# Kernel optimization log

Measured on AMD Instinct MI355X. Metric: run time of the kernel, lower is better.

The kernel has to match this reference:

```python
import jax, jax.numpy as jnp
import numpy as np

LN_EPS = 1e-5
COS_EPS2 = 1e-16  # torch cosine_similarity: (n1*n2).clamp_min(eps**2), eps=1e-8


def _ln(x, g, b):
    m = jnp.mean(x, -1, keepdims=True)
    v = jnp.mean((x - m) ** 2, -1, keepdims=True)
    return (x - m) * jax.lax.rsqrt(v + LN_EPS) * g + b


def _span_pool(x, starts, ends, word_length):
    # x: [B, S, D] (text_feat[:, 1:]); spans pooled into slots 1..S of a [B, S+1, D] buffer
    B, S, D = x.shape
    cs = jnp.concatenate([jnp.zeros((B, 1, D), x.dtype), jnp.cumsum(x, axis=1)], axis=1)  # [B, S+1, D]
    pool = (jnp.take_along_axis(cs, ends[..., None], axis=1)
            - jnp.take_along_axis(cs, starts[..., None], axis=1))  # [B, S, D]
    mask = (jnp.arange(S)[None, :] < word_length[:, None]).astype(x.dtype)[..., None]
    return jnp.pad(pool * mask, ((0, 0), (1, 0), (0, 0)))  # [B, S+1, D], slot 0 = zeros


def _forward(text_hidden, vit_feature, pooler_out, target_mask, adj,
             ln_g, ln_b, wq, wk, wv, fc_w, mha_ln_g, mha_ln_b,
             w1a, b1a, w1b, b1b, w2a, b2a, w2b, b2b,
             loc_w, loc_b, out_w, out_b, word_length, tran_indices):
    B, L, D = text_hidden.shape
    H = wq.shape[1] // D  # n_head=4, d_k=d_v=768

    # eval mode: all dropouts are identity
    text_feat = _ln(text_hidden, ln_g, ln_b)

    # MultiHeadAttention(text_feat, vit, vit)
    q = (text_feat @ wq).reshape(B, L, H, D)
    k = (vit_feature @ wk).reshape(B, -1, H, D)
    v = (vit_feature @ wv).reshape(B, -1, H, D)
    attn = jnp.einsum('blhd,bmhd->bhlm', q, k) / jnp.sqrt(jnp.asarray(D, text_feat.dtype))
    attn = jax.nn.softmax(attn, axis=-1)
    ctx = jnp.einsum('bhlm,bmhd->blhd', attn, v).reshape(B, L, H * D)
    text_include_img = _ln(ctx @ fc_w + text_feat, mha_ln_g, mha_ln_b)

    # pairwise cosine similarity over sequence positions: [B, L, L]
    n = jnp.linalg.norm(text_include_img, axis=-1)
    sim = jnp.einsum('bld,bmd->blm', text_include_img, text_include_img)
    sim = sim / jnp.maximum(n[:, :, None] * n[:, None, :], COS_EPS2)

    global_bert = _ln(pooler_out, ln_g, ln_b)

    # span pooling of subword features into word slots (tmps buffers)
    starts, ends = tran_indices[..., 0], tran_indices[..., 1]
    tmps = _span_pool(text_feat[:, 1:, :], starts, ends, word_length)
    tmps_ti = _span_pool(text_include_img[:, 1:, :], starts, ends, word_length)

    adj_ti = adj * sim
    den = jnp.sum(adj, axis=2, keepdims=True) + 1.0
    den_ti = jnp.sum(adj_ti, axis=2, keepdims=True) + 1.0

    # NOTE: original loop recomputes from tmps each layer and only keeps the last
    # iteration, so only W1[-1]/W2[-1] affect the output (faithfully reproduced).
    g_dep = jax.nn.relu(((adj @ tmps) @ w1b + b1b) / den)
    g_ti = jax.nn.relu(((adj_ti @ tmps_ti) @ w2b + b2b) / den_ti)

    asp_wn = jnp.sum(target_mask, axis=1, keepdims=True)  # [B, 1]
    m = target_mask[:, :, None]
    gcn_out_text = jnp.sum(g_dep * m, axis=1) / asp_wn
    gcn_out_ti = jnp.sum(g_ti * m, axis=1) / asp_wn

    local_feat = jnp.concatenate([gcn_out_text, gcn_out_ti], axis=1) @ loc_w + loc_b
    feat = jnp.concatenate([global_bert, local_feat], axis=1)
    return feat @ out_w + out_b


def setup_inputs():
    key = jax.random.key(0)
    ks = jax.random.split(key, 20)
    B, L, NV, D, H, NC = 64, 160, 197, 768, 4, 3
    S = L - 1
    s = 0.02
    text_hidden = jax.random.normal(ks[0], (B, L, D), jnp.float32)
    vit_feature = jax.random.normal(ks[1], (B, NV, D), jnp.float32)
    pooler_out = jax.random.normal(ks[2], (B, D), jnp.float32)
    adj = jax.random.uniform(ks[3], (B, L, L), jnp.float32)
    target_mask = jnp.zeros((B, L), jnp.float32).at[:, 1:9].set(1.0)
    word_length = jax.random.randint(ks[4], (B,), 1, S, jnp.int32)
    lens = jax.random.randint(ks[5], (B, S), 1, 3, jnp.int32)  # 1-2 subtokens per word
    cum = jnp.cumsum(lens, axis=1)
    ends = jnp.minimum(cum, S)
    starts = jnp.minimum(cum - lens, S)
    tran_indices = jnp.stack([starts, ends], axis=-1).astype(jnp.int32)
    return dict(
        text_hidden=text_hidden, vit_feature=vit_feature, pooler_out=pooler_out,
        target_mask=target_mask, adj=adj,
        ln_g=jnp.ones((D,), jnp.float32), ln_b=jnp.zeros((D,), jnp.float32),
        wq=jax.random.normal(ks[6], (D, H * D), jnp.float32) * s,
        wk=jax.random.normal(ks[7], (D, H * D), jnp.float32) * s,
        wv=jax.random.normal(ks[8], (D, H * D), jnp.float32) * s,
        fc_w=jax.random.normal(ks[9], (H * D, D), jnp.float32) * s,
        mha_ln_g=jnp.ones((D,), jnp.float32), mha_ln_b=jnp.zeros((D,), jnp.float32),
        w1a=jax.random.normal(ks[10], (D, D), jnp.float32) * s, b1a=jnp.zeros((D,), jnp.float32),
        w1b=jax.random.normal(ks[11], (D, D), jnp.float32) * s, b1b=jnp.zeros((D,), jnp.float32),
        w2a=jax.random.normal(ks[12], (D, D), jnp.float32) * s, b2a=jnp.zeros((D,), jnp.float32),
        w2b=jax.random.normal(ks[13], (D, D), jnp.float32) * s, b2b=jnp.zeros((D,), jnp.float32),
        loc_w=jax.random.normal(ks[14], (2 * D, D), jnp.float32) * s, loc_b=jnp.zeros((D,), jnp.float32),
        out_w=jax.random.normal(ks[15], (2 * D, NC), jnp.float32) * s, out_b=jnp.zeros((NC,), jnp.float32),
        word_length=word_length, tran_indices=tran_indices,
    )


def reference(text_hidden, vit_feature, pooler_out, target_mask, adj,
              ln_g, ln_b, wq, wk, wv, fc_w, mha_ln_g, mha_ln_b,
              w1a, b1a, w1b, b1b, w2a, b2a, w2b, b2b,
              loc_w, loc_b, out_w, out_b, word_length, tran_indices):
    return _forward(text_hidden, vit_feature, pooler_out, target_mask, adj,
                    ln_g, ln_b, wq, wk, wv, fc_w, mha_ln_g, mha_ln_b,
                    w1a, b1a, w1b, b1b, w2a, b2a, w2b, b2b,
                    loc_w, loc_b, out_w, out_b, word_length, tran_indices)
```

## Files before the change

kernel.cpp:

```cpp
#include <hip/hip_runtime.h>
#include <math.h>

#define BB 64
#define LL 160
#define DD 768
#define HH 4
#define NVV 197
#define SS 159

typedef unsigned short u16;
typedef __attribute__((ext_vector_type(8))) short bf16x8;
typedef __attribute__((ext_vector_type(4))) float f32x4;

union QU { uint4 u; bf16x8 v; };

__device__ __forceinline__ u16 f2bf(float a) {
  unsigned u = __builtin_bit_cast(unsigned, a);
  u = (u + 0x7FFFu + ((u >> 16) & 1u)) >> 16;
  return (u16)u;
}
__device__ __forceinline__ unsigned f2bf2(float a, float b) {
  return (unsigned)f2bf(a) | ((unsigned)f2bf(b) << 16);
}
__device__ __forceinline__ float bf2f(u16 h) {
  unsigned u = ((unsigned)h) << 16;
  return __builtin_bit_cast(float, u);
}
__device__ __forceinline__ float to_f(float x) { return x; }
__device__ __forceinline__ float to_f(u16 x) { return bf2f(x); }

__device__ __forceinline__ void async16(const u16* g, void* l) {
  __builtin_amdgcn_global_load_lds(
      (const __attribute__((address_space(1))) void*)g,
      (__attribute__((address_space(3))) void*)l, 16, 0, 0);
}

__device__ __forceinline__ uint4 load_bf8(const u16* __restrict__ P, long long rowbase,
                                          int valid, int kb, int K) {
  uint4 r;
  if (valid && (kb + 8 <= K) && (((rowbase + kb) & 7) == 0)) {
    r = *(const uint4*)(P + rowbase + kb);
  } else {
    u16 e[8];
    #pragma unroll
    for (int i = 0; i < 8; ++i) { int k = kb + i; e[i] = (valid && k < K) ? P[rowbase + k] : (u16)0; }
    r.x = e[0] | ((unsigned)e[1] << 16); r.y = e[2] | ((unsigned)e[3] << 16);
    r.z = e[4] | ((unsigned)e[5] << 16); r.w = e[6] | ((unsigned)e[7] << 16);
  }
  return r;
}

__device__ __forceinline__ uint4 load_row8(const float* __restrict__ P, long long rowbase,
                                           int valid_row, int kb, int K) {
  float f[8];
  if (valid_row && (kb + 8 <= K)) {
    const float4* p0 = (const float4*)(P + rowbase + kb);
    float4 x = p0[0], y = p0[1];
    f[0] = x.x; f[1] = x.y; f[2] = x.z; f[3] = x.w;
    f[4] = y.x; f[5] = y.y; f[6] = y.z; f[7] = y.w;
  } else {
    #pragma unroll
    for (int e = 0; e < 8; ++e) { int k = kb + e; f[e] = (valid_row && k < K) ? P[rowbase + k] : 0.f; }
  }
  uint4 r;
  r.x = f2bf2(f[0], f[1]); r.y = f2bf2(f[2], f[3]);
  r.z = f2bf2(f[4], f[5]); r.w = f2bf2(f[6], f[7]);
  return r;
}

__device__ __forceinline__ uint4 load_a(const u16* P, long long rb, int v, int kb, int K) {
  return load_bf8(P, rb, v, kb, K);
}
__device__ __forceinline__ uint4 load_a(const float* P, long long rb, int v, int kb, int K) {
  return load_row8(P, rb, v, kb, K);
}

template<int DUAL>
__global__ __launch_bounds__(256) void gemm97(
    const u16* __restrict__ A0, const u16* __restrict__ B0m,
    float* __restrict__ Cf0, u16* __restrict__ Cb0,
    const u16* __restrict__ A1, const u16* __restrict__ B1m,
    float* __restrict__ Cf1, u16* __restrict__ Cb1,
    int M, int N, int K, int lda, int ldb, int ldc, int nbx,
    const float* __restrict__ bias0, const float* __restrict__ bias1,
    const u16* __restrict__ resid0,
    const float* __restrict__ rowdiv0, const float* __restrict__ rowdiv1,
    int relu) {
  __shared__ uint4 Al[2][4][128];
  __shared__ uint4 Bl[2][4][128];

  int id = blockIdx.x;
  int nset = gridDim.x >> DUAL;
  int setid = DUAL ? (id >= nset ? 1 : 0) : 0;
  if (setid) id -= nset;
  const u16* A = setid ? A1 : A0;
  const u16* Bm = setid ? B1m : B0m;
  float* Cf = setid ? Cf1 : Cf0;
  u16* Cb = setid ? Cb1 : Cb0;
  const float* bias = setid ? bias1 : bias0;
  const float* rowdiv = setid ? rowdiv1 : rowdiv0;
  const u16* residB = setid ? (const u16*)nullptr : resid0;

  int qq = nset >> 3, rr = nset & 7;
  int xcd = id & 7, idx = id >> 3;
  int swz = (xcd < rr ? xcd * (qq + 1) : rr * (qq + 1) + (xcd - rr) * qq) + idx;
  int bx = swz % nbx, by = swz / nbx;
  int row0 = by * 128, col0 = bx * 128;

  int t = threadIdx.x, l = t & 63, w = t >> 6;
  int wr = (w >> 1) * 64, wc = (w & 1) * 64;
  int li = l & 15, kg = l >> 4;
  int nt = K >> 5;

  const u16* Ap0 = A + (long long)(row0 + l) * lda + w * 8;
  const u16* Ap1 = A + (long long)(row0 + 64 + l) * lda + w * 8;
  const u16* Bp0 = Bm + (long long)(col0 + l) * ldb + w * 8;
  const u16* Bp1 = Bm + (long long)(col0 + 64 + l) * ldb + w * 8;

  f32x4 acc[4][4] = {};

  auto STAGE = [&](int kt, int bi) {
    long long ko = (long long)kt << 5;
    async16(Ap0 + ko, &Al[bi][w][0]);
    async16(Ap1 + ko, &Al[bi][w][64]);
    async16(Bp0 + ko, &Bl[bi][w][0]);
    async16(Bp1 + ko, &Bl[bi][w][64]);
  };

  STAGE(0, 0);
  __syncthreads();
  int buf = 0;
  for (int kt = 0; kt < nt; ++kt) {
    if (kt + 1 < nt) STAGE(kt + 1, buf ^ 1);
    QU a[4], b[4];
    #pragma unroll
    for (int i = 0; i < 4; ++i) a[i].u = Al[buf][kg][wr + i * 16 + li];
    #pragma unroll
    for (int j = 0; j < 4; ++j) b[j].u = Bl[buf][kg][wc + j * 16 + li];
    __builtin_amdgcn_s_setprio(1);
    #pragma unroll
    for (int i = 0; i < 4; ++i)
      #pragma unroll
      for (int j = 0; j < 4; ++j)
        acc[i][j] = __builtin_amdgcn_mfma_f32_16x16x32_bf16(a[i].v, b[j].v, acc[i][j], 0, 0, 0);
    __builtin_amdgcn_s_setprio(0);
    __syncthreads();
    buf ^= 1;
  }

  #pragma unroll
  for (int i = 0; i < 4; ++i)
    #pragma unroll
    for (int j = 0; j < 4; ++j) {
      int col = col0 + wc + j * 16 + li;
      float bv = bias ? bias[col] : 0.f;
      #pragma unroll
      for (int r = 0; r < 4; ++r) {
        int row = row0 + wr + i * 16 + kg * 4 + r;
        long long ci = (long long)row * ldc + col;
        float v = acc[i][j][r] + bv;
        if (residB) v += bf2f(residB[ci]);
        if (rowdiv) v /= rowdiv[row];
        if (relu) v = fmaxf(v, 0.f);
        if (Cf) Cf[ci] = v;
        if (Cb) Cb[ci] = f2bf(v);
      }
    }
}

template<bool TRANSB, typename TA>
__global__ __launch_bounds__(256) void gemm_bf16(
    const TA* __restrict__ A, const u16* __restrict__ Bm,
    float* __restrict__ Cf, u16* __restrict__ Cb,
    int M, int N, int K, int lda, int ldb, int ldc, int Hb,
    long long sAb, long long sAh, long long sBb, long long sBh,
    long long sCb, long long sCh,
    float alpha, const float* __restrict__ bias) {
  int bb = blockIdx.z / Hb, hh = blockIdx.z % Hb;
  A += bb * sAb + hh * sAh;
  Bm += bb * sBb + hh * sBh;
  long long coff = bb * sCb + hh * sCh;

  __shared__ uint4 As4[4][64];
  __shared__ uint4 Bs4[4][64];

  int row0 = blockIdx.y * 64, col0 = blockIdx.x * 64;
  int t = threadIdx.x;
  int l = t & 63, w = t >> 6;
  int mq = (w >> 1) * 32, nq = (w & 1) * 32;

  int am = t >> 2, akq = t & 3;
  int bn = t & 63, bkq = t >> 6;

  f32x4 acc[2][2] = {};

  for (int k0 = 0; k0 < K; k0 += 32) {
    As4[akq][am] = load_a(A, (long long)(row0 + am) * lda, (row0 + am) < M, k0 + akq * 8, K);
    if (TRANSB) {
      Bs4[akq][am] = load_bf8(Bm, (long long)(col0 + am) * ldb, (col0 + am) < N, k0 + akq * 8, K);
    } else {
      int gn = col0 + bn;
      u16 e[8];
      #pragma unroll
      for (int i = 0; i < 8; ++i) {
        int k = k0 + bkq * 8 + i;
        e[i] = (gn < N && k < K) ? Bm[(long long)k * ldb + gn] : (u16)0;
      }
      uint4 r;
      r.x = e[0] | ((unsigned)e[1] << 16); r.y = e[2] | ((unsigned)e[3] << 16);
      r.z = e[4] | ((unsigned)e[5] << 16); r.w = e[6] | ((unsigned)e[7] << 16);
      Bs4[bkq][bn] = r;
    }
    __syncthreads();
    int kg = l >> 4, li = l & 15;
    QU a0, a1, b0, b1;
    a0.u = As4[kg][mq + li];
    a1.u = As4[kg][mq + 16 + li];
    b0.u = Bs4[kg][nq + li];
    b1.u = Bs4[kg][nq + 16 + li];
    acc[0][0] = __builtin_amdgcn_mfma_f32_16x16x32_bf16(a0.v, b0.v, acc[0][0], 0, 0, 0);
    acc[0][1] = __builtin_amdgcn_mfma_f32_16x16x32_bf16(a0.v, b1.v, acc[0][1], 0, 0, 0);
    acc[1][0] = __builtin_amdgcn_mfma_f32_16x16x32_bf16(a1.v, b0.v, acc[1][0], 0, 0, 0);
    acc[1][1] = __builtin_amdgcn_mfma_f32_16x16x32_bf16(a1.v, b1.v, acc[1][1], 0, 0, 0);
    __syncthreads();
  }

  #pragma unroll
  for (int i = 0; i < 2; ++i) {
    #pragma unroll
    for (int j = 0; j < 2; ++j) {
      int colj = col0 + nq + j * 16 + (l & 15);
      float bv = (bias && colj < N) ? bias[colj] : 0.f;
      #pragma unroll
      for (int r = 0; r < 4; ++r) {
        int gr = row0 + mq + i * 16 + (l >> 4) * 4 + r;
        if (gr < M && colj < N) {
          long long ci = coff + (long long)gr * ldc + colj;
          float v = acc[i][j][r] * alpha + bv;
          if (Cf) Cf[ci] = v;
          if (Cb) Cb[ci] = f2bf(v);
        }
      }
    }
  }
}

__global__ __launch_bounds__(256) void sim_kernel(
    const u16* __restrict__ TII, const float* __restrict__ nrm,
    const float* __restrict__ adjf, u16* __restrict__ adjtiB) {
  int bb = blockIdx.z;
  const u16* T = TII + (long long)bb * LL * DD;

  __shared__ uint4 As4[4][64];
  __shared__ uint4 Bs4[4][64];

  int row0 = blockIdx.y * 64, col0 = blockIdx.x * 64;
  int t = threadIdx.x;
  int l = t & 63, w = t >> 6;
  int mq = (w >> 1) * 32, nq = (w & 1) * 32;
  int am = t >> 2, akq = t & 3;

  f32x4 acc[2][2] = {};

  for (int k0 = 0; k0 < DD; k0 += 32) {
    As4[akq][am] = load_bf8(T, (long long)(row0 + am) * DD, (row0 + am) < LL, k0 + akq * 8, DD);
    Bs4[akq][am] = load_bf8(T, (long long)(col0 + am) * DD, (col0 + am) < LL, k0 + akq * 8, DD);
    __syncthreads();
    int kg = l >> 4, li = l & 15;
    QU a0, a1, b0, b1;
    a0.u = As4[kg][mq + li];
    a1.u = As4[kg][mq + 16 + li];
    b0.u = Bs4[kg][nq + li];
    b1.u = Bs4[kg][nq + 16 + li];
    acc[0][0] = __builtin_amdgcn_mfma_f32_16x16x32_bf16(a0.v, b0.v, acc[0][0], 0, 0, 0);
    acc[0][1] = __builtin_amdgcn_mfma_f32_16x16x32_bf16(a0.v, b1.v, acc[0][1], 0, 0, 0);
    acc[1][0] = __builtin_amdgcn_mfma_f32_16x16x32_bf16(a1.v, b0.v, acc[1][0], 0, 0, 0);
    acc[1][1] = __builtin_amdgcn_mfma_f32_16x16x32_bf16(a1.v, b1.v, acc[1][1], 0, 0, 0);
    __syncthreads();
  }

  #pragma unroll
  for (int i = 0; i < 2; ++i) {
    #pragma unroll
    for (int j = 0; j < 2; ++j) {
      int colj = col0 + nq + j * 16 + (l & 15);
      #pragma unroll
      for (int r = 0; r < 4; ++r) {
        int gr = row0 + mq + i * 16 + (l >> 4) * 4 + r;
        if (gr < LL && colj < LL) {
          float nl = nrm[bb * LL + gr], nm = nrm[bb * LL + colj];
          long long ai = ((long long)bb * LL + gr) * LL + colj;
          float s = acc[i][j][r] / fmaxf(nl * nm, 1e-16f);
          adjtiB[ai] = f2bf(adjf[ai] * s);
        }
      }
    }
  }
}

__device__ __forceinline__ float block_sum(float v, float* sm) {
  #pragma unroll
  for (int o = 32; o > 0; o >>= 1) v += __shfl_down(v, o);
  int lane = threadIdx.x & 63, w = threadIdx.x >> 6;
  if (lane == 0) sm[w] = v;
  __syncthreads();
  if (threadIdx.x == 0) sm[0] = sm[0] + sm[1] + sm[2] + sm[3];
  __syncthreads();
  float r = sm[0];
  __syncthreads();
  return r;
}

__global__ __launch_bounds__(256) void ln_kernel(const float* __restrict__ x, float* __restrict__ yf,
                                                 u16* __restrict__ yb,
                                                 const float* __restrict__ g, const float* __restrict__ b,
                                                 float* __restrict__ nrmout) {
  __shared__ float sm[4];
  long long row = blockIdx.x;
  const float* xr = x + row * DD;
  int t = threadIdx.x;
  float v0 = xr[t], v1 = xr[t + 256], v2 = xr[t + 512];
  float s = block_sum(v0 + v1 + v2, sm);
  float m = s * (1.f / 768.f);
  float d0 = v0 - m, d1 = v1 - m, d2 = v2 - m;
  float vv = block_sum(d0 * d0 + d1 * d1 + d2 * d2, sm);
  float rstd = rsqrtf(vv * (1.f / 768.f) + 1e-5f);
  float y0 = d0 * rstd * g[t] + b[t];
  float y1 = d1 * rstd * g[t + 256] + b[t + 256];
  float y2 = d2 * rstd * g[t + 512] + b[t + 512];
  if (yf) { float* yr = yf + row * DD; yr[t] = y0; yr[t + 256] = y1; yr[t + 512] = y2; }
  if (yb) { u16* yr = yb + row * DD; yr[t] = f2bf(y0); yr[t + 256] = f2bf(y1); yr[t + 512] = f2bf(y2); }
  if (nrmout) {
    float s2 = block_sum(y0 * y0 + y1 * y1 + y2 * y2, sm);
    if (t == 0) nrmout[row] = sqrtf(s2);
  }
}

__global__ __launch_bounds__(256) void softmax_bf16(u16* __restrict__ SP, int nrows) {
  int row = blockIdx.x * 4 + (threadIdx.x >> 6);
  int lane = threadIdx.x & 63;
  if (row >= nrows) return;
  u16* ar = SP + (long long)row * 200;
  float vals[4];
  float mx = -1e30f;
  int cnt = 0;
  for (int i = lane; i < NVV; i += 64) { float v = bf2f(ar[i]); vals[cnt++] = v; mx = fmaxf(mx, v); }
  #pragma unroll
  for (int o = 32; o > 0; o >>= 1) mx = fmaxf(mx, __shfl_xor(mx, o));
  float sum = 0.f;
  for (int j = 0; j < cnt; ++j) { vals[j] = __expf(vals[j] - mx); sum += vals[j]; }
  #pragma unroll
  for (int o = 32; o > 0; o >>= 1) sum += __shfl_xor(sum, o);
  float inv = 1.f / sum;
  cnt = 0;
  for (int i = lane; i < NVV; i += 64) ar[i] = f2bf(vals[cnt++] * inv);
  for (int i = NVV + lane; i < 200; i += 64) ar[i] = 0;
}

template<typename T>
__global__ __launch_bounds__(256) void pool_kernel(const T* __restrict__ src, u16* __restrict__ dst,
                                                   const int* __restrict__ wl, const int* __restrict__ tran) {
  int b = blockIdx.x, i = blockIdx.y, d = threadIdx.x;
  long long ob = ((long long)b * LL + i) * DD;
  float r0 = 0.f, r1 = 0.f, r2 = 0.f;
  if (i > 0 && (i - 1) < wl[b]) {
    int w = i - 1;
    int st = tran[(b * SS + w) * 2];
    int en = tran[(b * SS + w) * 2 + 1];
    const T* sb = src + (long long)b * LL * DD;
    for (int s = st; s < en; ++s) {
      const T* rp = sb + (long long)(1 + s) * DD;
      r0 += to_f(rp[d]); r1 += to_f(rp[d + 256]); r2 += to_f(rp[d + 512]);
    }
  }
  dst[ob + d] = f2bf(r0);
  dst[ob + d + 256] = f2bf(r1);
  dst[ob + d + 512] = f2bf(r2);
}

__global__ __launch_bounds__(256) void den_kernel(const float* __restrict__ adjf, const u16* __restrict__ atB,
                                                  float* __restrict__ den, float* __restrict__ den_ti) {
  __shared__ float sm[4];
  int bl = blockIdx.x, m = threadIdx.x;
  float a = 0.f, at = 0.f;
  if (m < LL) {
    long long idx = (long long)bl * LL + m;
    a = adjf[idx];
    at = bf2f(atB[idx]);
  }
  float sa = block_sum(a, sm);
  float sat = block_sum(at, sm);
  if (m == 0) { den[bl] = sa + 1.f; den_ti[bl] = sat + 1.f; }
}

__global__ __launch_bounds__(256) void gcn_kernel(const u16* __restrict__ g, const float* __restrict__ mask,
                                                  u16* __restrict__ outB, int coloff) {
  int b = blockIdx.x;
  int d = blockIdx.y * 256 + threadIdx.x;
  float s = 0.f, wn = 0.f;
  for (int l = 0; l < LL; ++l) {
    float mk = mask[b * LL + l];
    wn += mk;
    s += mk * bf2f(g[((long long)b * LL + l) * DD + d]);
  }
  outB[(long long)b * (2 * DD) + coloff + d] = f2bf(s / wn);
}

__global__ __launch_bounds__(256) void final_kernel(const float* __restrict__ gb, const float* __restrict__ lf,
                                                    const float* __restrict__ ow, const float* __restrict__ ob,
                                                    float* __restrict__ out) {
  __shared__ float sm[4];
  int b = blockIdx.x / 3, c = blockIdx.x % 3;
  int t = threadIdx.x;
  float s = 0.f;
  for (int k = t; k < DD; k += 256) {
    s += gb[b * DD + k] * ow[k * 3 + c];
    s += lf[b * DD + k] * ow[(DD + k) * 3 + c];
  }
  float tot = block_sum(s, sm);
  if (t == 0) out[b * 3 + c] = tot + ob[c];
}

__global__ __launch_bounds__(256) void conv_kernel(const float4* __restrict__ x, uint2* __restrict__ y, int n4) {
  int i = blockIdx.x * 256 + threadIdx.x;
  if (i < n4) {
    float4 v = x[i];
    uint2 o;
    o.x = f2bf2(v.x, v.y);
    o.y = f2bf2(v.z, v.w);
    y[i] = o;
  }
}

__global__ __launch_bounds__(256) void tconv_kernel(const float* __restrict__ src, u16* __restrict__ dst,
                                                    int R, int C, int lds, int ldd) {
  __shared__ float sm[32][33];
  int t = threadIdx.x;
  int tx = t & 31, ty8 = t >> 5;
  int r0 = blockIdx.y * 32, c0 = blockIdx.x * 32;
  for (int i = ty8; i < 32; i += 8) {
    int r = r0 + i, c = c0 + tx;
    sm[i][tx] = (r < R && c < C) ? src[(long long)r * lds + c] : 0.f;
  }
  __syncthreads();
  for (int i = ty8; i < 32; i += 8) {
    int c = c0 + i, r = r0 + tx;
    if (c < C && r < R) dst[(long long)c * ldd + r] = f2bf(sm[tx][i]);
  }
}

__global__ __launch_bounds__(256) void vtrans_kernel(const u16* __restrict__ src, u16* __restrict__ dst) {
  __shared__ u16 sm[32][33];
  int b = blockIdx.z;
  int c0 = blockIdx.x * 32;
  int r0 = blockIdx.y * 32;
  int t = threadIdx.x, tx = t & 31, ty8 = t >> 5;
  const u16* sb = src + (long long)b * NVV * DD;
  for (int i = ty8; i < 32; i += 8) {
    int r = r0 + i, c = c0 + tx;
    sm[i][tx] = (r < NVV && c < DD) ? sb[(long long)r * DD + c] : (u16)0;
  }
  __syncthreads();
  u16* db = dst + (long long)b * DD * 208;
  for (int i = ty8; i < 32; i += 8) {
    int j = c0 + i, k = r0 + tx;
    if (j < DD && k < 208) db[(long long)j * 208 + k] = sm[tx][i];
  }
}

template<typename TA>
static void gemm(hipStream_t s, bool transb, const TA* A, const u16* B, float* Cf, u16* Cb,
                 int M, int N, int K, int lda, int ldb, int ldc, int batches, int Hb,
                 long long sAb, long long sAh, long long sBb, long long sBh,
                 long long sCb, long long sCh, float alpha, const float* bias) {
  dim3 g((N + 63) / 64, (M + 63) / 64, batches);
  if (transb)
    gemm_bf16<true, TA><<<g, 256, 0, s>>>(A, B, Cf, Cb, M, N, K, lda, ldb, ldc, Hb,
                                          sAb, sAh, sBb, sBh, sCb, sCh, alpha, bias);
  else
    gemm_bf16<false, TA><<<g, 256, 0, s>>>(A, B, Cf, Cb, M, N, K, lda, ldb, ldc, Hb,
                                           sAb, sAh, sBb, sBh, sCb, sCh, alpha, bias);
}

extern "C" void kernel_launch(void* const* d_in, const int* in_sizes, int n_in,
                              void* d_out, int out_size, void* d_ws, size_t ws_size,
                              hipStream_t stream) {
  const float* text_hidden = (const float*)d_in[0];
  const float* vit_feature = (const float*)d_in[1];
  const float* pooler_out = (const float*)d_in[2];
  const float* target_mask = (const float*)d_in[3];
  const float* adj = (const float*)d_in[4];
  const float* ln_g = (const float*)d_in[5];
  const float* ln_b = (const float*)d_in[6];
  const float* wq = (const float*)d_in[7];
  const float* wk = (const float*)d_in[8];
  const float* wv = (const float*)d_in[9];
  const float* fc_w = (const float*)d_in[10];
  const float* mha_ln_g = (const float*)d_in[11];
  const float* mha_ln_b = (const float*)d_in[12];
  const float* w1b = (const float*)d_in[15];
  const float* b1b = (const float*)d_in[16];
  const float* w2b = (const float*)d_in[19];
  const float* b2b = (const float*)d_in[20];
  const float* loc_w = (const float*)d_in[21];
  const float* loc_b = (const float*)d_in[22];
  const float* out_w = (const float*)d_in[23];
  const float* out_b = (const float*)d_in[24];
  const int* word_length = (const int*)d_in[25];
  const int* tran = (const int*)d_in[26];
  float* out = (float*)d_out;

  const long long BLD = (long long)BB * LL * DD;
  const long long BND = (long long)BB * NVV * DD;
  const long long WHD = (long long)768 * 768;
  const long long W3K = (long long)768 * 3072;

  char* base = (char*)d_ws;
  auto alloc = [&](size_t bytes) { char* p = base; base += (bytes + 255) & ~(size_t)255; return p; };

  float* R_ACC = (float*)alloc(BLD * 4);
  u16* TFB = (u16*)alloc(BLD * 2);
  u16* vitB = (u16*)alloc(BND * 2);
  u16* BIG = (u16*)alloc((size_t)4 * BLD * 2);
  u16* Mt = (u16*)alloc((size_t)4 * WHD * 2);
  u16* Wvf = (u16*)alloc((size_t)4 * WHD * 2);
  u16* SH = (u16*)alloc((size_t)BB * HH * LL * 200 * 2);
  u16* adjtiB = (u16*)alloc((size_t)BB * LL * LL * 2);
  u16* w1bT = (u16*)alloc(WHD * 2);
  u16* w2bT = (u16*)alloc(WHD * 2);
  u16* locT = (u16*)alloc((size_t)768 * 1536 * 2);
  u16* linB = (u16*)alloc((size_t)BB * 1536 * 2);
  float* nrm = (float*)alloc((size_t)BB * LL * 4);
  float* den = (float*)alloc((size_t)BB * LL * 4);
  float* den_ti = (float*)alloc((size_t)BB * LL * 4);
  float* global_bert = (float*)alloc((size_t)BB * DD * 4);
  float* local_feat = (float*)alloc((size_t)BB * DD * 4);

  u16* wqB = BIG;
  u16* wkB = BIG + W3K;
  u16* wvB = BIG + 2 * W3K;
  u16* fcT = BIG + 3 * W3K;
  u16* T2PV = BIG;
  u16* TIIB = BIG + 2 * BLD;
  u16* tmpsTiB = BIG;
  u16* g2B = BIG + BLD;
  u16* S4 = SH;
  u16* H1 = SH;
  u16* tmpsB = vitB;
  u16* h2B = TFB;
  u16* g1B = vitB;
  u16* vitT = (u16*)R_ACC;

  const float inv_sqrt_d = 1.0f / sqrtf((float)DD);
  const long long sA_L = (long long)LL * DD;

  {
    int n4v = (int)(BND / 4);
    conv_kernel<<<(n4v + 255) / 256, 256, 0, stream>>>((const float4*)vit_feature, (uint2*)vitB, n4v);
    vtrans_kernel<<<dim3(24, 7, BB), 256, 0, stream>>>(vitB, vitT);
    int n4w = (int)(W3K / 4);
    conv_kernel<<<(n4w + 255) / 256, 256, 0, stream>>>((const float4*)wq, (uint2*)wqB, n4w);
    conv_kernel<<<(n4w + 255) / 256, 256, 0, stream>>>((const float4*)wk, (uint2*)wkB, n4w);
    conv_kernel<<<(n4w + 255) / 256, 256, 0, stream>>>((const float4*)wv, (uint2*)wvB, n4w);
    for (int h = 0; h < HH; ++h)
      tconv_kernel<<<dim3(24, 24), 256, 0, stream>>>(fc_w + (size_t)h * WHD, fcT + (size_t)h * WHD,
                                                     768, 768, 768, 768);
    tconv_kernel<<<dim3(24, 24), 256, 0, stream>>>(w1b, w1bT, 768, 768, 768, 768);
    tconv_kernel<<<dim3(24, 24), 256, 0, stream>>>(w2b, w2bT, 768, 768, 768, 768);
    tconv_kernel<<<dim3(24, 48), 256, 0, stream>>>(loc_w, locT, 1536, 768, 768, 1536);
    gemm<u16>(stream, true, wkB, wqB, nullptr, Mt, 768, 768, 768, 3072, 3072, 768,
              HH, 1, 768, 0, 768, 0, WHD, 0, 1.f, nullptr);
    gemm<u16>(stream, true, fcT, wvB, nullptr, Wvf, 768, 768, 768, 768, 3072, 3072,
              HH, 1, WHD, 0, 768, 0, 768, 0, 1.f, nullptr);
  }

  ln_kernel<<<BB * LL, 256, 0, stream>>>(text_hidden, nullptr, TFB, ln_g, ln_b, nullptr);
  gemm97<0><<<1920, 256, 0, stream>>>(TFB, Mt, nullptr, T2PV,
                                      nullptr, nullptr, nullptr, nullptr,
                                      BB * LL, 4 * DD, DD, DD, DD, 4 * DD, 24,
                                      nullptr, nullptr, nullptr, nullptr, nullptr, 0);
  gemm<u16>(stream, true, T2PV, vitB, nullptr, S4, LL, NVV, DD, 4 * DD, DD, 200,
            BB * HH, HH, (long long)LL * 4 * DD, DD, (long long)NVV * DD, 0,
            (long long)HH * LL * 200, (long long)LL * 200, inv_sqrt_d, nullptr);
  softmax_bf16<<<(BB * HH * LL + 3) / 4, 256, 0, stream>>>(S4, BB * HH * LL);
  gemm<u16>(stream, true, S4, vitT, nullptr, T2PV, LL, DD, NVV, 200, 208, 4 * DD,
            BB * HH, HH, (long long)HH * LL * 200, (long long)LL * 200,
            (long long)DD * 208, 0, (long long)LL * 4 * DD, DD, 1.f, nullptr);
  gemm97<0><<<480, 256, 0, stream>>>(T2PV, Wvf, R_ACC, nullptr,
                                     nullptr, nullptr, nullptr, nullptr,
                                     BB * LL, DD, 4 * DD, 4 * DD, 4 * DD, DD, 6,
                                     nullptr, nullptr, TFB, nullptr, nullptr, 0);

  ln_kernel<<<BB * LL, 256, 0, stream>>>(R_ACC, nullptr, TIIB, mha_ln_g, mha_ln_b, nrm);
  sim_kernel<<<dim3(3, 3, BB), 256, 0, stream>>>(TIIB, nrm, adj, adjtiB);
  den_kernel<<<BB * LL, 256, 0, stream>>>(adj, adjtiB, den, den_ti);
  pool_kernel<u16><<<dim3(BB, LL), 256, 0, stream>>>(TFB, tmpsB, word_length, tran);
  pool_kernel<u16><<<dim3(BB, LL), 256, 0, stream>>>(TIIB, tmpsTiB, word_length, tran);
  gemm<float>(stream, false, adj, tmpsB, nullptr, H1, LL, DD, LL, LL, DD, DD,
              BB, 1, (long long)LL * LL, 0, sA_L, 0, sA_L, 0, 1.f, nullptr);
  gemm<u16>(stream, false, adjtiB, tmpsTiB, nullptr, h2B, LL, DD, LL, LL, DD, DD,
            BB, 1, (long long)LL * LL, 0, sA_L, 0, sA_L, 0, 1.f, nullptr);
  gemm97<1><<<960, 256, 0, stream>>>(H1, w1bT, nullptr, g1B,
                                     h2B, w2bT, nullptr, g2B,
                                     BB * LL, DD, DD, DD, DD, DD, 6,
                                     b1b, b2b, nullptr, den, den_ti, 1);
  gcn_kernel<<<dim3(BB, 3), 256, 0, stream>>>(g1B, target_mask, linB, 0);
  gcn_kernel<<<dim3(BB, 3), 256, 0, stream>>>(g2B, target_mask, linB, DD);
  ln_kernel<<<BB, 256, 0, stream>>>(pooler_out, global_bert, nullptr, ln_g, ln_b, nullptr);
  gemm<u16>(stream, true, linB, locT, local_feat, nullptr, BB, DD, 2 * DD, 2 * DD, 2 * DD, DD,
            1, 1, 0, 0, 0, 0, 0, 0, 1.f, loc_b);
  final_kernel<<<BB * 3, 256, 0, stream>>>(global_bert, local_feat, out_w, out_b, out);
}
```

Baseline: 752.4 us.

## Add single-wave async-copy bf16 GEMM for attention batched matmuls, pad K to 224

Adds a 64-thread, 64x64-tile bf16 MFMA GEMM that double-buffers 32-wide K slices into shared memory with async copies. It replaces the generic gemm_bf16 for the weight-product precomputes and for the two per-head attention GEMMs (scores and probs times V). The score and V-transposed buffers are padded from 200/208 to 224 columns so K is a multiple of 32 without bounds checks. The 1/sqrt(d) scale moves from the score GEMM into the precomputed Wk·Wq product. The padding adds memory traffic and zero work, and the single-wave blocks may leave occupancy or latency hiding lower.

```diff
diff --git a/kernel.cpp b/kernel.cpp
--- a/kernel.cpp
+++ b/kernel.cpp
@@ -7,6 +7,7 @@
 #define HH 4
 #define NVV 197
 #define SS 159
+#define KP 224
 
 typedef unsigned short u16;
 typedef __attribute__((ext_vector_type(8))) short bf16x8;
@@ -73,6 +74,81 @@
 }
 __device__ __forceinline__ uint4 load_a(const float* P, long long rb, int v, int kb, int K) {
   return load_row8(P, rb, v, kb, K);
+}
+
+__global__ __launch_bounds__(64) void gemm_bt1(
+    const u16* __restrict__ A, const u16* __restrict__ Bm,
+    float* __restrict__ Cf, u16* __restrict__ Cb,
+    int M, int N, int K, int lda, int ldb, int ldc, int Hb,
+    long long sAb, long long sAh, long long sBb, long long sBh,
+    long long sCb, long long sCh, float alpha) {
+  __shared__ uint4 Al[2][4][64];
+  __shared__ uint4 Bl[2][4][64];
+
+  int z = blockIdx.z;
+  int bb = z / Hb, hh = z % Hb;
+  A += bb * sAb + hh * sAh;
+  Bm += bb * sBb + hh * sBh;
+  long long coff = bb * sCb + hh * sCh;
+
+  int row0 = blockIdx.y * 64, col0 = blockIdx.x * 64;
+  int l = threadIdx.x;
+  int li = l & 15, kg = l >> 4;
+  int nt = K >> 5;
+
+  int ra = row0 + l; if (ra > M - 1) ra = M - 1;
+  int rb = col0 + l; if (rb > N - 1) rb = N - 1;
+  const u16* Ap = A + (long long)ra * lda;
+  const u16* Bp = Bm + (long long)rb * ldb;
+
+  f32x4 acc[4][4] = {};
+
+  auto STG = [&](int kt, int bi) {
+    long long ko = (long long)kt << 5;
+    #pragma unroll
+    for (int s = 0; s < 4; ++s) {
+      async16(Ap + ko + s * 8, &Al[bi][s][0]);
+      async16(Bp + ko + s * 8, &Bl[bi][s][0]);
+    }
+  };
+
+  STG(0, 0);
+  __syncthreads();
+  int buf = 0;
+  for (int kt = 0; kt < nt; ++kt) {
+    if (kt + 1 < nt) STG(kt + 1, buf ^ 1);
+    QU a[4], b[4];
+    #pragma unroll
+    for (int i = 0; i < 4; ++i) a[i].u = Al[buf][kg][i * 16 + li];
+    #pragma unroll
+    for (int j = 0; j < 4; ++j) b[j].u = Bl[buf][kg][j * 16 + li];
+    __builtin_amdgcn_s_setprio(1);
+    #pragma unroll
+    for (int i = 0; i < 4; ++i)
+      #pragma unroll
+      for (int j = 0; j < 4; ++j)
+        acc[i][j] = __builtin_amdgcn_mfma_f32_16x16x32_bf16(a[i].v, b[j].v, acc[i][j], 0, 0, 0);
+    __builtin_amdgcn_s_setprio(0);
+    __syncthreads();
+    buf ^= 1;
+  }
+
+  #pragma unroll
+  for (int i = 0; i < 4; ++i)
+    #pragma unroll
+    for (int j = 0; j < 4; ++j) {
+      int col = col0 + j * 16 + li;
+      #pragma unroll
+      for (int r = 0; r < 4; ++r) {
+        int row = row0 + i * 16 + kg * 4 + r;
+        if (row < M && col < N) {
+          long long ci = coff + (long long)row * ldc + col;
+          float v = acc[i][j][r] * alpha;
+          if (Cf) Cf[ci] = v;
+          if (Cb) Cb[ci] = f2bf(v);
+        }
+      }
+    }
 }
 
 template<int DUAL>
@@ -340,7 +416,7 @@
   int row = blockIdx.x * 4 + (threadIdx.x >> 6);
   int lane = threadIdx.x & 63;
   if (row >= nrows) return;
-  u16* ar = SP + (long long)row * 200;
+  u16* ar = SP + (long long)row * KP;
   float vals[4];
   float mx = -1e30f;
   int cnt = 0;
@@ -354,7 +430,7 @@
   float inv = 1.f / sum;
   cnt = 0;
   for (int i = lane; i < NVV; i += 64) ar[i] = f2bf(vals[cnt++] * inv);
-  for (int i = NVV + lane; i < 200; i += 64) ar[i] = 0;
+  for (int i = NVV + lane; i < KP; i += 64) ar[i] = 0;
 }
 
 template<typename T>
@@ -461,10 +537,10 @@
     sm[i][tx] = (r < NVV && c < DD) ? sb[(long long)r * DD + c] : (u16)0;
   }
   __syncthreads();
-  u16* db = dst + (long long)b * DD * 208;
+  u16* db = dst + (long long)b * DD * KP;
   for (int i = ty8; i < 32; i += 8) {
     int j = c0 + i, k = r0 + tx;
-    if (j < DD && k < 208) db[(long long)j * 208 + k] = sm[tx][i];
+    if (j < DD && k < KP) db[(long long)j * KP + k] = sm[tx][i];
   }
 }
 
@@ -480,6 +556,15 @@
   else
     gemm_bf16<false, TA><<<g, 256, 0, s>>>(A, B, Cf, Cb, M, N, K, lda, ldb, ldc, Hb,
                                            sAb, sAh, sBb, sBh, sCb, sCh, alpha, bias);
+}
+
+static void gemm_bt1h(hipStream_t s, const u16* A, const u16* B, float* Cf, u16* Cb,
+                      int M, int N, int K, int lda, int ldb, int ldc, int batches, int Hb,
+                      long long sAb, long long sAh, long long sBb, long long sBh,
+                      long long sCb, long long sCh, float alpha) {
+  dim3 g((N + 63) / 64, (M + 63) / 64, batches);
+  gemm_bt1<<<g, 64, 0, s>>>(A, B, Cf, Cb, M, N, K, lda, ldb, ldc, Hb,
+                            sAb, sAh, sBb, sBh, sCb, sCh, alpha);
 }
 
 extern "C" void kernel_launch(void* const* d_in, const int* in_sizes, int n_in,
@@ -524,7 +609,7 @@
   u16* BIG = (u16*)alloc((size_t)4 * BLD * 2);
   u16* Mt = (u16*)alloc((size_t)4 * WHD * 2);
   u16* Wvf = (u16*)alloc((size_t)4 * WHD * 2);
-  u16* SH = (u16*)alloc((size_t)BB * HH * LL * 200 * 2);
+  u16* SH = (u16*)alloc((size_t)BB * HH * LL * KP * 2);
   u16* adjtiB = (u16*)alloc((size_t)BB * LL * LL * 2);
   u16* w1bT = (u16*)alloc(WHD * 2);
   u16* w2bT = (u16*)alloc(WHD * 2);
@@ -568,10 +653,10 @@
     tconv_kernel<<<dim3(24, 24), 256, 0, stream>>>(w1b, w1bT, 768, 768, 768, 768);
     tconv_kernel<<<dim3(24, 24), 256, 0, stream>>>(w2b, w2bT, 768, 768, 768, 768);
     tconv_kernel<<<dim3(24, 48), 256, 0, stream>>>(loc_w, locT, 1536, 768, 768, 1536);
-    gemm<u16>(stream, true, wkB, wqB, nullptr, Mt, 768, 768, 768, 3072, 3072, 768,
-              HH, 1, 768, 0, 768, 0, WHD, 0, 1.f, nullptr);
-    gemm<u16>(stream, true, fcT, wvB, nullptr, Wvf, 768, 768, 768, 768, 3072, 3072,
-              HH, 1, WHD, 0, 768, 0, 768, 0, 1.f, nullptr);
+    gemm_bt1h(stream, wkB, wqB, nullptr, Mt, 768, 768, 768, 3072, 3072, 768,
+              HH, HH, 0, 768, 0, 768, 0, WHD, inv_sqrt_d);
+    gemm_bt1h(stream, fcT, wvB, nullptr, Wvf, 768, 768, 768, 768, 3072, 3072,
+              HH, HH, 0, WHD, 0, 768, 0, 768, 1.f);
   }
 
   ln_kernel<<<BB * LL, 256, 0, stream>>>(text_hidden, nullptr, TFB, ln_g, ln_b, nullptr);
@@ -579,13 +664,13 @@
                                       nullptr, nullptr, nullptr, nullptr,
                                       BB * LL, 4 * DD, DD, DD, DD, 4 * DD, 24,
                                       nullptr, nullptr, nullptr, nullptr, nullptr, 0);
-  gemm<u16>(stream, true, T2PV, vitB, nullptr, S4, LL, NVV, DD, 4 * DD, DD, 200,
+  gemm_bt1h(stream, T2PV, vitB, nullptr, S4, LL, NVV, DD, 4 * DD, DD, KP,
             BB * HH, HH, (long long)LL * 4 * DD, DD, (long long)NVV * DD, 0,
-            (long long)HH * LL * 200, (long long)LL * 200, inv_sqrt_d, nullptr);
+            (long long)HH * LL * KP, (long long)LL * KP, 1.f);
   softmax_bf16<<<(BB * HH * LL + 3) / 4, 256, 0, stream>>>(S4, BB * HH * LL);
-  gemm<u16>(stream, true, S4, vitT, nullptr, T2PV, LL, DD, NVV, 200, 208, 4 * DD,
-            BB * HH, HH, (long long)HH * LL * 200, (long long)LL * 200,
-            (long long)DD * 208, 0, (long long)LL * 4 * DD, DD, 1.f, nullptr);
+  gemm_bt1h(stream, S4, vitT, nullptr, T2PV, LL, DD, KP, KP, KP, 4 * DD,
+            BB * HH, HH, (long long)HH * LL * KP, (long long)LL * KP,
+            (long long)DD * KP, 0, (long long)LL * 4 * DD, DD, 1.f);
   gemm97<0><<<480, 256, 0, stream>>>(T2PV, Wvf, R_ACC, nullptr,
                                      nullptr, nullptr, nullptr, nullptr,
                                      BB * LL, DD, 4 * DD, 4 * DD, 4 * DD, DD, 6,
```

New measurement: 878.7 us. 16.8% more time.
